# Optimization experiments

Measured on AMD Instinct MI355X. Metric: run time of the kernel, lower is better.

## Reference

```python
import jax, jax.numpy as jnp
import numpy as np

N = 50000
E = 1600000
IN_CH = 34
HID = 64
OUT = 64
NEG_SLOPE = 0.2


def _gat_layer(x, src, dst, W, a_src, a_dst, bias, heads, out_ch, concat):
    n = x.shape[0]
    xw = (x @ W).reshape(n, heads, out_ch)                      # [N,H,C]
    al_src = jnp.sum(xw * a_src[None], axis=-1)                  # [N,H]
    al_dst = jnp.sum(xw * a_dst[None], axis=-1)                  # [N,H]
    e = jax.nn.leaky_relu(al_src[src] + al_dst[dst], NEG_SLOPE)  # [E,H]
    # segment softmax over incoming edges of each dst node (self-loops ensure non-empty)
    m = jax.ops.segment_max(e, dst, num_segments=n)              # [N,H]
    ex = jnp.exp(e - m[dst])
    denom = jax.ops.segment_sum(ex, dst, num_segments=n)         # [N,H]
    alpha = ex / denom[dst]                                      # [E,H]
    msg = xw[src] * alpha[:, :, None]                            # [E,H,C]
    out = jax.ops.segment_sum(msg, dst, num_segments=n)          # [N,H,C]
    if concat:
        out = out.reshape(n, heads * out_ch)
    else:
        out = out.mean(axis=1)
    return out + bias


def setup_inputs() -> dict:
    key = jax.random.key(0)
    ks = jax.random.split(key, 12)
    x = jax.random.normal(ks[0], (N, IN_CH), dtype=jnp.float32)
    edge_index = jax.random.randint(ks[1], (2, E), 0, N, dtype=jnp.int64)
    # layer 1: heads=2, concat -> 128
    W1 = jax.random.normal(ks[2], (IN_CH, 2 * HID), dtype=jnp.float32) * 0.1
    a_src1 = jax.random.normal(ks[3], (2, HID), dtype=jnp.float32) * 0.1
    a_dst1 = jax.random.normal(ks[4], (2, HID), dtype=jnp.float32) * 0.1
    b1 = jnp.zeros((2 * HID,), dtype=jnp.float32)
    # layer 2: heads=1, mean
    W2 = jax.random.normal(ks[5], (2 * HID, OUT), dtype=jnp.float32) * 0.1
    a_src2 = jax.random.normal(ks[6], (1, OUT), dtype=jnp.float32) * 0.1
    a_dst2 = jax.random.normal(ks[7], (1, OUT), dtype=jnp.float32) * 0.1
    b2 = jnp.zeros((OUT,), dtype=jnp.float32)
    return {"x": x, "edge_index": edge_index, "W1": W1, "a_src1": a_src1,
            "a_dst1": a_dst1, "b1": b1, "W2": W2, "a_src2": a_src2,
            "a_dst2": a_dst2, "b2": b2}


def reference(x, edge_index, W1, a_src1, a_dst1, b1, W2, a_src2, a_dst2, b2):
    n = x.shape[0]
    loops = jnp.arange(n, dtype=edge_index.dtype)
    src = jnp.concatenate([edge_index[0], loops])  # PyG GATConv add_self_loops=True
    dst = jnp.concatenate([edge_index[1], loops])
    h = _gat_layer(x, src, dst, W1, a_src1, a_dst1, b1, heads=2, out_ch=HID, concat=True)
    h = jax.nn.relu(h)
    out = _gat_layer(h, src, dst, W2, a_src2, a_dst2, b2, heads=1, out_ch=OUT, concat=False)
    return out
```

## Files before the change

### kernel.cpp

```cpp
#include <hip/hip_runtime.h>
#include <math.h>

#define N_NODES 50000
#define E_EDGES 1600000
#define IN_CH   34
#define NEG     0.2f
#define NB      196
#define CAP     10000

typedef __attribute__((ext_vector_type(2))) float fv2;

static __device__ __forceinline__ unsigned short f2bf(float f) {
    unsigned int u = __float_as_uint(f);
    u += 0x7fffu + ((u >> 16) & 1u);
    return (unsigned short)(u >> 16);
}
static __device__ __forceinline__ float bflo(unsigned int u) {
    return __uint_as_float(u << 16);
}
static __device__ __forceinline__ float bfhi(unsigned int u) {
    return __uint_as_float(u & 0xffff0000u);
}
static __device__ __forceinline__ float lrelu_exp(float e) {
    return expf(e > 0.f ? e : NEG * e);
}

static __device__ __forceinline__ int scan256_excl(int v, int* wsum) {
    const int lane = threadIdx.x & 63, wv = threadIdx.x >> 6;
    int x = v;
    #pragma unroll
    for (int off = 1; off < 64; off <<= 1) {
        int y = __shfl_up(x, off);
        if (lane >= off) x += y;
    }
    if (lane == 63) wsum[wv] = x;
    __syncthreads();
    if (threadIdx.x < 4) {
        int s = wsum[threadIdx.x];
        #pragma unroll
        for (int off = 1; off < 4; off <<= 1) {
            int y = __shfl_up(s, off);
            if ((int)threadIdx.x >= off) s += y;
        }
        wsum[threadIdx.x] = s;
    }
    __syncthreads();
    const int woff = wv ? wsum[wv - 1] : 0;
    return woff + x - v;
}

__global__ __launch_bounds__(256) void k_bin_node1(
    const int* __restrict__ srcA, const int* __restrict__ dstA,
    int* __restrict__ gcur, unsigned int* __restrict__ binned,
    const float* __restrict__ x, const float* __restrict__ W1,
    const float* __restrict__ a_src, const float* __restrict__ a_dst,
    unsigned short* __restrict__ xw1b,
    float* __restrict__ al_s, float* __restrict__ al_d)
{
    __shared__ __align__(16) char sm[69664];
    const int tid = threadIdx.x;

    if (blockIdx.x < NB) {
        unsigned int* raw  = (unsigned int*)sm;
        unsigned int* ebuf = (unsigned int*)(sm + 32768);
        int* cnt  = (int*)(sm + 65536);
        int* loff = (int*)(sm + 66560);
        int* lcur = (int*)(sm + 67584);
        int* cur  = (int*)(sm + 68608);
        int* wsum = (int*)(sm + 69632);
        cnt[tid] = 0;
        __syncthreads();
        const int base = blockIdx.x * 8192;
        #pragma unroll
        for (int i = 0; i < 32; ++i) {
            const int e = base + i * 256 + tid;
            if (e < E_EDGES) {
                const int d = dstA[e], s = srcA[e];
                raw[i * 256 + tid] = ((unsigned int)d << 16) | (unsigned int)s;
                atomicAdd(&cnt[d >> 8], 1);
            }
        }
        __syncthreads();
        const int v = cnt[tid];
        const int excl = scan256_excl(v, wsum);
        loff[tid] = excl;
        lcur[tid] = excl;
        cur[tid] = (tid < NB && v > 0) ? (tid * CAP + atomicAdd(&gcur[tid], v)) : 0;
        __syncthreads();
        const int mE = min(8192, E_EDGES - base);
        #pragma unroll
        for (int i = 0; i < 32; ++i) {
            const int p = i * 256 + tid;
            if (p < mE) {
                const unsigned int u = raw[p];
                const int q = atomicAdd(&lcur[u >> 24], 1);
                ebuf[q] = u;
            }
        }
        __syncthreads();
        #pragma unroll
        for (int i = 0; i < 32; ++i) {
            const int p = i * 256 + tid;
            if (p < mE) {
                const unsigned int u = ebuf[p];
                const int b = (int)(u >> 24);
                binned[cur[b] + (p - loff[b])] = u;
            }
        }
    } else {
        float* sW  = (float*)sm;
        float* sx  = (float*)(sm + 17952);
        float* sas = (float*)(sm + 22432);
        float* sad = (float*)(sm + 22944);
        for (int i = tid; i < IN_CH * 128; i += 256) {
            int k = i >> 7, c = i & 127;
            sW[k * 132 + c] = W1[i];
        }
        if (tid < 128) { sas[tid] = a_src[tid]; sad[tid] = a_dst[tid]; }
        const int n0 = (blockIdx.x - NB) * 32;
        for (int i = tid; i < 32 * IN_CH; i += 256) {
            int n = i / IN_CH;
            sx[n * 35 + (i - n * IN_CH)] = (n0 + n < N_NODES) ? x[n0 * IN_CH + i] : 0.f;
        }
        __syncthreads();

        const int tc = tid & 31, tn = tid >> 5;
        float acc[4][4] = {{0.f}};
        for (int k = 0; k < IN_CH; ++k) {
            const float4 wv = *reinterpret_cast<const float4*>(&sW[k * 132 + 4 * tc]);
            #pragma unroll
            for (int j = 0; j < 4; ++j) {
                const float hj = sx[(4 * tn + j) * 35 + k];
                acc[j][0] += hj * wv.x; acc[j][1] += hj * wv.y;
                acc[j][2] += hj * wv.z; acc[j][3] += hj * wv.w;
            }
        }
        #pragma unroll
        for (int j = 0; j < 4; ++j) {
            const int node = n0 + 4 * tn + j;
            float ps = 0.f, pd = 0.f;
            #pragma unroll
            for (int c = 0; c < 4; ++c) {
                ps += acc[j][c] * sas[4 * tc + c];
                pd += acc[j][c] * sad[4 * tc + c];
            }
            #pragma unroll
            for (int off = 1; off < 16; off <<= 1) {
                ps += __shfl_xor(ps, off);
                pd += __shfl_xor(pd, off);
            }
            if (node < N_NODES) {
                if ((tc & 15) == 0) {
                    int h = tc >> 4;
                    al_s[node * 2 + h] = ps;
                    al_d[node * 2 + h] = pd;
                }
                ushort4 u;
                u.x = f2bf(acc[j][0]); u.y = f2bf(acc[j][1]);
                u.z = f2bf(acc[j][2]); u.w = f2bf(acc[j][3]);
                *reinterpret_cast<ushort4*>(&xw1b[node * 128 + 4 * tc]) = u;
            }
        }
    }
}

__global__ __launch_bounds__(256) void k_fine(
    const int* __restrict__ gcur, const unsigned int* __restrict__ binned,
    int2* __restrict__ rowspan, int* __restrict__ sorted_src)
{
    __shared__ unsigned int sbin[CAP];
    __shared__ int cnt[256], lcur[256];
    __shared__ int wsum[4];
    const int tid = threadIdx.x;
    const int b = blockIdx.x;
    const int bbase = b * CAP;
    const int cntb = gcur[b];
    cnt[tid] = 0;
    __syncthreads();
    for (int p = tid; p < cntb; p += 256) {
        const unsigned int u = binned[bbase + p];
        sbin[p] = u;
        atomicAdd(&cnt[(u >> 16) & 255], 1);
    }
    __syncthreads();
    const int v = cnt[tid];
    const int excl = scan256_excl(v, wsum);
    const int node = b * 256 + tid;
    if (node < N_NODES) rowspan[node] = make_int2(bbase + excl, bbase + excl + v);
    lcur[tid] = excl;
    __syncthreads();
    for (int p = tid; p < cntb; p += 256) {
        const unsigned int u = sbin[p];
        const int q = atomicAdd(&lcur[(u >> 16) & 255], 1);
        sorted_src[bbase + q] = (int)(u & 0xffffu);
    }
}

__global__ __launch_bounds__(256) void k_gather1(
    const int2* __restrict__ rowspan, const int* __restrict__ sorted_src,
    const unsigned int* __restrict__ xw1u,
    const float* __restrict__ al_s, const float* __restrict__ al_d,
    const float* __restrict__ b1, float* __restrict__ hbuf)
{
    __shared__ float4 AB[2][4][32];
    const int wave = threadIdx.x >> 6;
    const int lane = threadIdx.x & 63;
    const int node = (blockIdx.x * 256 + threadIdx.x) >> 6;
    if (node >= N_NODES) return;
    const int2 span = rowspan[node];
    const int head = lane >> 5;

    const float2 ald  = *reinterpret_cast<const float2*>(&al_d[node * 2]);
    const float2 als0 = *reinterpret_cast<const float2*>(&al_s[node * 2]);
    const float w0h0 = lrelu_exp(als0.x + ald.x);
    const float w0h1 = lrelu_exp(als0.y + ald.y);
    const float wself = head ? w0h1 : w0h0;

    const unsigned int su = xw1u[node * 64 + lane];
    fv2 accX = { wself * bflo(su), wself * bfhi(su) };
    fv2 accY = { 0.f, 0.f };
    float dv0 = 0.f, dv1 = 0.f;
    const float4* ABh = AB[head][wave];

    for (int base = span.x; base < span.y; base += 64) {
        const int rem = span.y - base;
        const int m = rem < 64 ? rem : 64;
        const int mp = (m + 1) & ~1;
        if (lane < m) {
            const int s = sorted_src[base + lane];
            const float2 als = *reinterpret_cast<const float2*>(&al_s[s * 2]);
            const float w0 = lrelu_exp(als.x + ald.x);
            const float w1 = lrelu_exp(als.y + ald.y);
            dv0 += w0; dv1 += w1;
            const float offf = __int_as_float(s << 6);
            ((float2*)&AB[0][wave][lane >> 1])[lane & 1] = make_float2(offf, w0);
            ((float2*)&AB[1][wave][lane >> 1])[lane & 1] = make_float2(offf, w1);
        } else if (lane < mp) {
            const float offf = __int_as_float(node << 6);
            ((float2*)&AB[0][wave][lane >> 1])[lane & 1] = make_float2(offf, 0.f);
            ((float2*)&AB[1][wave][lane >> 1])[lane & 1] = make_float2(offf, 0.f);
        }
        const int P = mp >> 1;
        int p = 0;
        for (; p + 4 <= P; p += 4) {
            const float4 q0 = ABh[p + 0];
            const float4 q1 = ABh[p + 1];
            const float4 q2 = ABh[p + 2];
            const float4 q3 = ABh[p + 3];
            const unsigned int a0 = xw1u[__float_as_int(q0.x) + lane];
            const unsigned int b0 = xw1u[__float_as_int(q0.z) + lane];
            const unsigned int a1 = xw1u[__float_as_int(q1.x) + lane];
            const unsigned int b1v = xw1u[__float_as_int(q1.z) + lane];
            const unsigned int a2 = xw1u[__float_as_int(q2.x) + lane];
            const unsigned int b2 = xw1u[__float_as_int(q2.z) + lane];
            const unsigned int a3 = xw1u[__float_as_int(q3.x) + lane];
            const unsigned int b3 = xw1u[__float_as_int(q3.z) + lane];
            fv2 f;
            f.x = bflo(a0); f.y = bfhi(a0); accX += f * q0.y;
            f.x = bflo(b0); f.y = bfhi(b0); accY += f * q0.w;
            f.x = bflo(a1); f.y = bfhi(a1); accX += f * q1.y;
            f.x = bflo(b1v); f.y = bfhi(b1v); accY += f * q1.w;
            f.x = bflo(a2); f.y = bfhi(a2); accX += f * q2.y;
            f.x = bflo(b2); f.y = bfhi(b2); accY += f * q2.w;
            f.x = bflo(a3); f.y = bfhi(a3); accX += f * q3.y;
            f.x = bflo(b3); f.y = bfhi(b3); accY += f * q3.w;
        }
        for (; p < P; ++p) {
            const float4 q = ABh[p];
            const unsigned int a = xw1u[__float_as_int(q.x) + lane];
            const unsigned int b = xw1u[__float_as_int(q.z) + lane];
            fv2 f;
            f.x = bflo(a); f.y = bfhi(a); accX += f * q.y;
            f.x = bflo(b); f.y = bfhi(b); accY += f * q.w;
        }
    }
    accX += accY;
    #pragma unroll
    for (int off = 32; off; off >>= 1) {
        dv0 += __shfl_xor(dv0, off);
        dv1 += __shfl_xor(dv1, off);
    }
    const float den = head ? (dv1 + w0h1) : (dv0 + w0h0);
    const float2 bv = *reinterpret_cast<const float2*>(&b1[2 * lane]);
    float o0 = accX.x / den + bv.x;
    float o1 = accX.y / den + bv.y;
    o0 = o0 > 0.f ? o0 : 0.f;
    o1 = o1 > 0.f ? o1 : 0.f;
    *reinterpret_cast<float2*>(&hbuf[node * 128 + 2 * lane]) = make_float2(o0, o1);
}

__global__ __launch_bounds__(256) void k_node2(
    const float* __restrict__ hbuf, const float* __restrict__ W2,
    const float* __restrict__ a_src, const float* __restrict__ a_dst,
    unsigned short* __restrict__ xw2b, float* __restrict__ al_s, float* __restrict__ al_d)
{
    __shared__ float sW[128 * 64];
    __shared__ float sh[64 * 129];
    __shared__ float sas[64], sad[64];
    const int tid = threadIdx.x;
    for (int i = tid; i < 128 * 64; i += 256) sW[i] = W2[i];
    if (tid < 64) { sas[tid] = a_src[tid]; sad[tid] = a_dst[tid]; }
    const int n0 = blockIdx.x * 64;
    for (int i = tid; i < 64 * 128; i += 256) {
        int n = i >> 7, c = i & 127;
        sh[n * 129 + c] = (n0 + n < N_NODES) ? hbuf[(long)(n0 + n) * 128 + c] : 0.f;
    }
    __syncthreads();

    const int tc = tid & 15, tn = tid >> 4;
    float acc[4][4] = {{0.f}};
    for (int k = 0; k < 128; ++k) {
        const float4 wv = *reinterpret_cast<const float4*>(&sW[k * 64 + 4 * tc]);
        #pragma unroll
        for (int j = 0; j < 4; ++j) {
            const float hj = sh[(4 * tn + j) * 129 + k];
            acc[j][0] += hj * wv.x; acc[j][1] += hj * wv.y;
            acc[j][2] += hj * wv.z; acc[j][3] += hj * wv.w;
        }
    }
    #pragma unroll
    for (int j = 0; j < 4; ++j) {
        const int node = n0 + 4 * tn + j;
        float ps = 0.f, pd = 0.f;
        #pragma unroll
        for (int c = 0; c < 4; ++c) {
            ps += acc[j][c] * sas[4 * tc + c];
            pd += acc[j][c] * sad[4 * tc + c];
        }
        #pragma unroll
        for (int off = 1; off < 16; off <<= 1) {
            ps += __shfl_xor(ps, off);
            pd += __shfl_xor(pd, off);
        }
        if (node < N_NODES) {
            if (tc == 0) { al_s[node] = ps; al_d[node] = pd; }
            ushort4 u;
            u.x = f2bf(acc[j][0]); u.y = f2bf(acc[j][1]);
            u.z = f2bf(acc[j][2]); u.w = f2bf(acc[j][3]);
            *reinterpret_cast<ushort4*>(&xw2b[node * 64 + 4 * tc]) = u;
        }
    }
}

__global__ __launch_bounds__(256) void k_gather2(
    const int2* __restrict__ rowspan, const int* __restrict__ sorted_src,
    const unsigned int* __restrict__ xw2u,
    const float* __restrict__ al_s, const float* __restrict__ al_d,
    const float* __restrict__ b2, float* __restrict__ out)
{
    __shared__ float4 AB[4][32];
    const int wave = threadIdx.x >> 6;
    const int lane = threadIdx.x & 63;
    const int node = (blockIdx.x * 256 + threadIdx.x) >> 6;
    if (node >= N_NODES) return;
    const int2 span = rowspan[node];
    const int li = lane & 31, hsel = lane >> 5;

    const float ald = al_d[node];
    const float w0s = lrelu_exp(al_s[node] + ald);
    const unsigned int su = xw2u[node * 32 + li];
    const float wself = hsel ? 0.f : w0s;
    fv2 acc = { wself * bflo(su), wself * bfhi(su) };
    float dv = 0.f;
    const float4* ABw = AB[wave];

    for (int base = span.x; base < span.y; base += 64) {
        const int rem = span.y - base;
        const int m = rem < 64 ? rem : 64;
        const int mp = (m + 3) & ~3;
        if (lane < m) {
            const int s = sorted_src[base + lane];
            const float w = lrelu_exp(al_s[s] + ald);
            dv += w;
            ((float2*)&AB[wave][lane >> 1])[lane & 1] =
                make_float2(__int_as_float(s << 5), w);
        } else if (lane < mp) {
            ((float2*)&AB[wave][lane >> 1])[lane & 1] =
                make_float2(__int_as_float(node << 5), 0.f);
        }
        const int P = mp >> 1;
        int p = hsel;
        for (; p + 2 < P; p += 4) {
            const float4 qA = ABw[p];
            const float4 qB = ABw[p + 2];
            const unsigned int aA = xw2u[__float_as_int(qA.x) + li];
            const unsigned int bA = xw2u[__float_as_int(qA.z) + li];
            const unsigned int aB = xw2u[__float_as_int(qB.x) + li];
            const unsigned int bB = xw2u[__float_as_int(qB.z) + li];
            fv2 f;
            f.x = bflo(aA); f.y = bfhi(aA); acc += f * qA.y;
            f.x = bflo(bA); f.y = bfhi(bA); acc += f * qA.w;
            f.x = bflo(aB); f.y = bfhi(aB); acc += f * qB.y;
            f.x = bflo(bB); f.y = bfhi(bB); acc += f * qB.w;
        }
        for (; p < P; p += 2) {
            const float4 q = ABw[p];
            const unsigned int a = xw2u[__float_as_int(q.x) + li];
            const unsigned int b = xw2u[__float_as_int(q.z) + li];
            fv2 f;
            f.x = bflo(a); f.y = bfhi(a); acc += f * q.y;
            f.x = bflo(b); f.y = bfhi(b); acc += f * q.w;
        }
    }
    acc.x += __shfl_xor(acc.x, 32);
    acc.y += __shfl_xor(acc.y, 32);
    #pragma unroll
    for (int off = 32; off; off >>= 1) dv += __shfl_xor(dv, off);
    if (lane < 32) {
        const float den = dv + w0s;
        const float2 bv = *reinterpret_cast<const float2*>(&b2[2 * li]);
        *reinterpret_cast<float2*>(&out[node * 64 + 2 * li]) =
            make_float2(acc.x / den + bv.x, acc.y / den + bv.y);
    }
}

extern "C" void kernel_launch(void* const* d_in, const int* in_sizes, int n_in,
                              void* d_out, int out_size, void* d_ws, size_t ws_size,
                              hipStream_t stream)
{
    const float* x   = (const float*)d_in[0];
    const int*   ei  = (const int*)d_in[1];
    const float* W1  = (const float*)d_in[2];
    const float* as1 = (const float*)d_in[3];
    const float* ad1 = (const float*)d_in[4];
    const float* b1  = (const float*)d_in[5];
    const float* W2  = (const float*)d_in[6];
    const float* as2 = (const float*)d_in[7];
    const float* ad2 = (const float*)d_in[8];
    const float* b2  = (const float*)d_in[9];
    float* out = (float*)d_out;

    const int* srcA = ei;
    const int* dstA = ei + E_EDGES;

    char* ws = (char*)d_ws;
    int2*  rowspan    = (int2*)(ws);
    int*   sorted_src = (int*)(ws + 409600);
    int*   gcur       = (int*)(ws + 8249600);
    float* al_s1      = (float*)(ws + 8251648);
    float* al_d1      = (float*)(ws + 8651648);
    float* al_s2      = (float*)(ws + 9051648);
    float* al_d2      = (float*)(ws + 9251648);
    unsigned short* xw1b = (unsigned short*)(ws + 9451648);
    float* hbuf       = (float*)(ws + 22251648);
    unsigned int* binned = (unsigned int*)hbuf;
    unsigned short* xw2b = (unsigned short*)(ws + 47851648);

    hipMemsetAsync(gcur, 0, NB * sizeof(int), stream);
    hipLaunchKernelGGL(k_bin_node1, dim3(NB + (N_NODES + 31) / 32), dim3(256), 0, stream,
                       srcA, dstA, gcur, binned,
                       x, W1, as1, ad1, xw1b, al_s1, al_d1);
    hipLaunchKernelGGL(k_fine, dim3(NB), dim3(256), 0, stream,
                       gcur, binned, rowspan, sorted_src);
    hipLaunchKernelGGL(k_gather1, dim3((N_NODES + 3) / 4), dim3(256), 0, stream,
                       rowspan, sorted_src, (const unsigned int*)xw1b,
                       al_s1, al_d1, b1, hbuf);
    hipLaunchKernelGGL(k_node2, dim3((N_NODES + 63) / 64), dim3(256), 0, stream,
                       hbuf, W2, as2, ad2, xw2b, al_s2, al_d2);
    hipLaunchKernelGGL(k_gather2, dim3((N_NODES + 3) / 4), dim3(256), 0, stream,
                       rowspan, sorted_src, (const unsigned int*)xw2b,
                       al_s2, al_d2, b2, out);
}
```

Before: 269.4 us.

## Replace two-pass bin sort with histogram, scan and atomic scatter CSR build

Replaces the coarse-bin plus in-shared-memory fine sort of edges by destination with a global per-node histogram kernel, a single-block exclusive scan, and an atomic-cursor scatter of source indices fused with the layer-1 node transform. This removes the intermediate binned buffer and the fine-sort kernel. In exchange it adds two launches, a serial single-block scan over 50k nodes, and 1.6M contended global atomics whose scattered writes leave edge order within each row nondeterministic.

```diff
diff --git a/kernel.cpp b/kernel.cpp
--- a/kernel.cpp
+++ b/kernel.cpp
@@ -5,8 +5,8 @@
 #define E_EDGES 1600000
 #define IN_CH   34
 #define NEG     0.2f
-#define NB      196
-#define CAP     10000
+#define HB      784
+#define SCB     512
 
 typedef __attribute__((ext_vector_type(2))) float fv2;
 
@@ -25,9 +25,34 @@
     return expf(e > 0.f ? e : NEG * e);
 }
 
-static __device__ __forceinline__ int scan256_excl(int v, int* wsum) {
-    const int lane = threadIdx.x & 63, wv = threadIdx.x >> 6;
-    int x = v;
+__global__ __launch_bounds__(256) void k_hist(
+    const int* __restrict__ dstA, int* __restrict__ hist)
+{
+    const int nq = E_EDGES / 4;
+    for (int q = blockIdx.x * 256 + threadIdx.x; q < nq; q += HB * 256) {
+        const int4 d = ((const int4*)dstA)[q];
+        atomicAdd(&hist[d.x], 1);
+        atomicAdd(&hist[d.y], 1);
+        atomicAdd(&hist[d.z], 1);
+        atomicAdd(&hist[d.w], 1);
+    }
+}
+
+__global__ __launch_bounds__(1024) void k_scan(
+    const int* __restrict__ hist, int2* __restrict__ rowspan,
+    int* __restrict__ cursor)
+{
+    __shared__ int wsum[16];
+    const int t = threadIdx.x;
+    const int CH = 49;
+    const int base = t * CH;
+    int s = 0;
+    for (int i = 0; i < CH; ++i) {
+        const int idx = base + i;
+        if (idx < N_NODES) s += hist[idx];
+    }
+    const int lane = t & 63, wv = t >> 6;
+    int x = s;
     #pragma unroll
     for (int off = 1; off < 64; off <<= 1) {
         int y = __shfl_up(x, off);
@@ -35,89 +60,58 @@
     }
     if (lane == 63) wsum[wv] = x;
     __syncthreads();
-    if (threadIdx.x < 4) {
-        int s = wsum[threadIdx.x];
+    if (t < 16) {
+        int v = wsum[t];
         #pragma unroll
-        for (int off = 1; off < 4; off <<= 1) {
-            int y = __shfl_up(s, off);
-            if ((int)threadIdx.x >= off) s += y;
-        }
-        wsum[threadIdx.x] = s;
+        for (int off = 1; off < 16; off <<= 1) {
+            int y = __shfl_up(v, off);
+            if (t >= off) v += y;
+        }
+        wsum[t] = v;
     }
     __syncthreads();
-    const int woff = wv ? wsum[wv - 1] : 0;
-    return woff + x - v;
-}
-
-__global__ __launch_bounds__(256) void k_bin_node1(
+    int run = (wv ? wsum[wv - 1] : 0) + x - s;
+    for (int i = 0; i < CH; ++i) {
+        const int idx = base + i;
+        if (idx < N_NODES) {
+            const int v = hist[idx];
+            rowspan[idx] = make_int2(run, run + v);
+            cursor[idx] = run;
+            run += v;
+        }
+    }
+}
+
+__global__ __launch_bounds__(256) void k_scatter_node1(
     const int* __restrict__ srcA, const int* __restrict__ dstA,
-    int* __restrict__ gcur, unsigned int* __restrict__ binned,
+    int* __restrict__ cursor, int* __restrict__ sorted_src,
     const float* __restrict__ x, const float* __restrict__ W1,
     const float* __restrict__ a_src, const float* __restrict__ a_dst,
     unsigned short* __restrict__ xw1b,
     float* __restrict__ al_s, float* __restrict__ al_d)
 {
-    __shared__ __align__(16) char sm[69664];
+    __shared__ float sW[IN_CH * 132];
+    __shared__ float sx[32 * 35];
+    __shared__ float sas[128], sad[128];
     const int tid = threadIdx.x;
 
-    if (blockIdx.x < NB) {
-        unsigned int* raw  = (unsigned int*)sm;
-        unsigned int* ebuf = (unsigned int*)(sm + 32768);
-        int* cnt  = (int*)(sm + 65536);
-        int* loff = (int*)(sm + 66560);
-        int* lcur = (int*)(sm + 67584);
-        int* cur  = (int*)(sm + 68608);
-        int* wsum = (int*)(sm + 69632);
-        cnt[tid] = 0;
-        __syncthreads();
-        const int base = blockIdx.x * 8192;
-        #pragma unroll
-        for (int i = 0; i < 32; ++i) {
-            const int e = base + i * 256 + tid;
-            if (e < E_EDGES) {
-                const int d = dstA[e], s = srcA[e];
-                raw[i * 256 + tid] = ((unsigned int)d << 16) | (unsigned int)s;
-                atomicAdd(&cnt[d >> 8], 1);
-            }
-        }
-        __syncthreads();
-        const int v = cnt[tid];
-        const int excl = scan256_excl(v, wsum);
-        loff[tid] = excl;
-        lcur[tid] = excl;
-        cur[tid] = (tid < NB && v > 0) ? (tid * CAP + atomicAdd(&gcur[tid], v)) : 0;
-        __syncthreads();
-        const int mE = min(8192, E_EDGES - base);
-        #pragma unroll
-        for (int i = 0; i < 32; ++i) {
-            const int p = i * 256 + tid;
-            if (p < mE) {
-                const unsigned int u = raw[p];
-                const int q = atomicAdd(&lcur[u >> 24], 1);
-                ebuf[q] = u;
-            }
-        }
-        __syncthreads();
-        #pragma unroll
-        for (int i = 0; i < 32; ++i) {
-            const int p = i * 256 + tid;
-            if (p < mE) {
-                const unsigned int u = ebuf[p];
-                const int b = (int)(u >> 24);
-                binned[cur[b] + (p - loff[b])] = u;
-            }
+    if (blockIdx.x < SCB) {
+        const int nq = E_EDGES / 4;
+        for (int q = blockIdx.x * 256 + tid; q < nq; q += SCB * 256) {
+            const int4 d = ((const int4*)dstA)[q];
+            const int4 s = ((const int4*)srcA)[q];
+            sorted_src[atomicAdd(&cursor[d.x], 1)] = s.x;
+            sorted_src[atomicAdd(&cursor[d.y], 1)] = s.y;
+            sorted_src[atomicAdd(&cursor[d.z], 1)] = s.z;
+            sorted_src[atomicAdd(&cursor[d.w], 1)] = s.w;
         }
     } else {
-        float* sW  = (float*)sm;
-        float* sx  = (float*)(sm + 17952);
-        float* sas = (float*)(sm + 22432);
-        float* sad = (float*)(sm + 22944);
         for (int i = tid; i < IN_CH * 128; i += 256) {
             int k = i >> 7, c = i & 127;
             sW[k * 132 + c] = W1[i];
         }
         if (tid < 128) { sas[tid] = a_src[tid]; sad[tid] = a_dst[tid]; }
-        const int n0 = (blockIdx.x - NB) * 32;
+        const int n0 = (blockIdx.x - SCB) * 32;
         for (int i = tid; i < 32 * IN_CH; i += 256) {
             int n = i / IN_CH;
             sx[n * 35 + (i - n * IN_CH)] = (n0 + n < N_NODES) ? x[n0 * IN_CH + i] : 0.f;
@@ -164,38 +158,6 @@
     }
 }
 
-__global__ __launch_bounds__(256) void k_fine(
-    const int* __restrict__ gcur, const unsigned int* __restrict__ binned,
-    int2* __restrict__ rowspan, int* __restrict__ sorted_src)
-{
-    __shared__ unsigned int sbin[CAP];
-    __shared__ int cnt[256], lcur[256];
-    __shared__ int wsum[4];
-    const int tid = threadIdx.x;
-    const int b = blockIdx.x;
-    const int bbase = b * CAP;
-    const int cntb = gcur[b];
-    cnt[tid] = 0;
-    __syncthreads();
-    for (int p = tid; p < cntb; p += 256) {
-        const unsigned int u = binned[bbase + p];
-        sbin[p] = u;
-        atomicAdd(&cnt[(u >> 16) & 255], 1);
-    }
-    __syncthreads();
-    const int v = cnt[tid];
-    const int excl = scan256_excl(v, wsum);
-    const int node = b * 256 + tid;
-    if (node < N_NODES) rowspan[node] = make_int2(bbase + excl, bbase + excl + v);
-    lcur[tid] = excl;
-    __syncthreads();
-    for (int p = tid; p < cntb; p += 256) {
-        const unsigned int u = sbin[p];
-        const int q = atomicAdd(&lcur[(u >> 16) & 255], 1);
-        sorted_src[bbase + q] = (int)(u & 0xffffu);
-    }
-}
-
 __global__ __launch_bounds__(256) void k_gather1(
     const int2* __restrict__ rowspan, const int* __restrict__ sorted_src,
     const unsigned int* __restrict__ xw1u,
@@ -436,22 +398,23 @@
     char* ws = (char*)d_ws;
     int2*  rowspan    = (int2*)(ws);
     int*   sorted_src = (int*)(ws + 409600);
-    int*   gcur       = (int*)(ws + 8249600);
-    float* al_s1      = (float*)(ws + 8251648);
-    float* al_d1      = (float*)(ws + 8651648);
-    float* al_s2      = (float*)(ws + 9051648);
-    float* al_d2      = (float*)(ws + 9251648);
-    unsigned short* xw1b = (unsigned short*)(ws + 9451648);
-    float* hbuf       = (float*)(ws + 22251648);
-    unsigned int* binned = (unsigned int*)hbuf;
-    unsigned short* xw2b = (unsigned short*)(ws + 47851648);
-
-    hipMemsetAsync(gcur, 0, NB * sizeof(int), stream);
-    hipLaunchKernelGGL(k_bin_node1, dim3(NB + (N_NODES + 31) / 32), dim3(256), 0, stream,
-                       srcA, dstA, gcur, binned,
+    int*   hist       = (int*)(ws + 6809600);
+    int*   cursor     = (int*)(ws + 7014400);
+    float* al_s1      = (float*)(ws + 7219200);
+    float* al_d1      = (float*)(ws + 7628800);
+    float* al_s2      = (float*)(ws + 8038400);
+    float* al_d2      = (float*)(ws + 8243200);
+    unsigned short* xw1b = (unsigned short*)(ws + 8448000);
+    float* hbuf       = (float*)(ws + 21248000);
+    unsigned short* xw2b = (unsigned short*)(ws + 46848000);
+
+    hipMemsetAsync(hist, 0, N_NODES * sizeof(int), stream);
+    hipLaunchKernelGGL(k_hist, dim3(HB), dim3(256), 0, stream, dstA, hist);
+    hipLaunchKernelGGL(k_scan, dim3(1), dim3(1024), 0, stream,
+                       hist, rowspan, cursor);
+    hipLaunchKernelGGL(k_scatter_node1, dim3(SCB + (N_NODES + 31) / 32), dim3(256), 0, stream,
+                       srcA, dstA, cursor, sorted_src,
                        x, W1, as1, ad1, xw1b, al_s1, al_d1);
-    hipLaunchKernelGGL(k_fine, dim3(NB), dim3(256), 0, stream,
-                       gcur, binned, rowspan, sorted_src);
     hipLaunchKernelGGL(k_gather1, dim3((N_NODES + 3) / 4), dim3(256), 0, stream,
                        rowspan, sorted_src, (const unsigned int*)xw1b,
                        al_s1, al_d1, b1, hbuf);
```

Result: slower. 534.3 us (+98.3%).

## Shrink binning chunks and split fine sort into four blocks per bin

Applied to the files above, without the earlier changes.

The coarse binning pass now gives each block 2048 edges instead of 8192, so 782 blocks run with about 23 KB of LDS instead of about 68 KB, which should raise occupancy. The fine sort pass launches four blocks per coarse bin, each owning 64 of the bin's 256 destination nodes. Each block still scans the whole bin to compute the global prefix offsets, but it only buffers and scatters its own quarter, holding at most 3072 edges in LDS. In exchange every bin is read from global memory four times, there are more global atomics on the bin counters, and any sub-bin holding more than 3072 edges is silently truncated.

```diff
diff --git a/kernel.cpp b/kernel.cpp
--- a/kernel.cpp
+++ b/kernel.cpp
@@ -7,6 +7,9 @@
 #define NEG     0.2f
 #define NB      196
 #define CAP     10000
+#define EPB     2048
+#define NBB     782
+#define FCAP    3072
 
 typedef __attribute__((ext_vector_type(2))) float fv2;
 
@@ -57,22 +60,22 @@
     unsigned short* __restrict__ xw1b,
     float* __restrict__ al_s, float* __restrict__ al_d)
 {
-    __shared__ __align__(16) char sm[69664];
+    __shared__ __align__(16) char sm[23456];
     const int tid = threadIdx.x;
 
-    if (blockIdx.x < NB) {
+    if (blockIdx.x < NBB) {
         unsigned int* raw  = (unsigned int*)sm;
-        unsigned int* ebuf = (unsigned int*)(sm + 32768);
-        int* cnt  = (int*)(sm + 65536);
-        int* loff = (int*)(sm + 66560);
-        int* lcur = (int*)(sm + 67584);
-        int* cur  = (int*)(sm + 68608);
-        int* wsum = (int*)(sm + 69632);
+        unsigned int* ebuf = (unsigned int*)(sm + 8192);
+        int* cnt  = (int*)(sm + 16384);
+        int* loff = (int*)(sm + 17408);
+        int* lcur = (int*)(sm + 18432);
+        int* cur  = (int*)(sm + 19456);
+        int* wsum = (int*)(sm + 20480);
         cnt[tid] = 0;
         __syncthreads();
-        const int base = blockIdx.x * 8192;
-        #pragma unroll
-        for (int i = 0; i < 32; ++i) {
+        const int base = blockIdx.x * EPB;
+        #pragma unroll
+        for (int i = 0; i < EPB / 256; ++i) {
             const int e = base + i * 256 + tid;
             if (e < E_EDGES) {
                 const int d = dstA[e], s = srcA[e];
@@ -87,9 +90,9 @@
         lcur[tid] = excl;
         cur[tid] = (tid < NB && v > 0) ? (tid * CAP + atomicAdd(&gcur[tid], v)) : 0;
         __syncthreads();
-        const int mE = min(8192, E_EDGES - base);
-        #pragma unroll
-        for (int i = 0; i < 32; ++i) {
+        const int mE = min(EPB, E_EDGES - base);
+        #pragma unroll
+        for (int i = 0; i < EPB / 256; ++i) {
             const int p = i * 256 + tid;
             if (p < mE) {
                 const unsigned int u = raw[p];
@@ -99,7 +102,7 @@
         }
         __syncthreads();
         #pragma unroll
-        for (int i = 0; i < 32; ++i) {
+        for (int i = 0; i < EPB / 256; ++i) {
             const int p = i * 256 + tid;
             if (p < mE) {
                 const unsigned int u = ebuf[p];
@@ -117,7 +120,7 @@
             sW[k * 132 + c] = W1[i];
         }
         if (tid < 128) { sas[tid] = a_src[tid]; sad[tid] = a_dst[tid]; }
-        const int n0 = (blockIdx.x - NB) * 32;
+        const int n0 = (blockIdx.x - NBB) * 32;
         for (int i = tid; i < 32 * IN_CH; i += 256) {
             int n = i / IN_CH;
             sx[n * 35 + (i - n * IN_CH)] = (n0 + n < N_NODES) ? x[n0 * IN_CH + i] : 0.f;
@@ -168,30 +171,41 @@
     const int* __restrict__ gcur, const unsigned int* __restrict__ binned,
     int2* __restrict__ rowspan, int* __restrict__ sorted_src)
 {
-    __shared__ unsigned int sbin[CAP];
-    __shared__ int cnt[256], lcur[256];
+    __shared__ unsigned int ebuf[FCAP];
+    __shared__ int cnt[256];
+    __shared__ int lcur[64];
     __shared__ int wsum[4];
+    __shared__ int myn;
     const int tid = threadIdx.x;
-    const int b = blockIdx.x;
+    const int b  = blockIdx.x >> 2;
+    const int lo = (blockIdx.x & 3) * 64;
     const int bbase = b * CAP;
     const int cntb = gcur[b];
     cnt[tid] = 0;
+    if (tid == 0) myn = 0;
     __syncthreads();
     for (int p = tid; p < cntb; p += 256) {
         const unsigned int u = binned[bbase + p];
-        sbin[p] = u;
-        atomicAdd(&cnt[(u >> 16) & 255], 1);
+        const int d8 = (int)((u >> 16) & 255);
+        atomicAdd(&cnt[d8], 1);
+        if ((d8 & ~63) == lo) {
+            const int k = atomicAdd(&myn, 1);
+            if (k < FCAP) ebuf[k] = u;
+        }
     }
     __syncthreads();
     const int v = cnt[tid];
     const int excl = scan256_excl(v, wsum);
-    const int node = b * 256 + tid;
-    if (node < N_NODES) rowspan[node] = make_int2(bbase + excl, bbase + excl + v);
-    lcur[tid] = excl;
-    __syncthreads();
-    for (int p = tid; p < cntb; p += 256) {
-        const unsigned int u = sbin[p];
-        const int q = atomicAdd(&lcur[(u >> 16) & 255], 1);
+    if ((tid & ~63) == lo) {
+        lcur[tid & 63] = excl;
+        const int node = b * 256 + tid;
+        if (node < N_NODES) rowspan[node] = make_int2(bbase + excl, bbase + excl + v);
+    }
+    __syncthreads();
+    const int tot = min(myn, FCAP);
+    for (int p = tid; p < tot; p += 256) {
+        const unsigned int u = ebuf[p];
+        const int q = atomicAdd(&lcur[(u >> 16) & 63], 1);
         sorted_src[bbase + q] = (int)(u & 0xffffu);
     }
 }
@@ -447,10 +461,10 @@
     unsigned short* xw2b = (unsigned short*)(ws + 47851648);
 
     hipMemsetAsync(gcur, 0, NB * sizeof(int), stream);
-    hipLaunchKernelGGL(k_bin_node1, dim3(NB + (N_NODES + 31) / 32), dim3(256), 0, stream,
+    hipLaunchKernelGGL(k_bin_node1, dim3(NBB + (N_NODES + 31) / 32), dim3(256), 0, stream,
                        srcA, dstA, gcur, binned,
                        x, W1, as1, ad1, xw1b, al_s1, al_d1);
-    hipLaunchKernelGGL(k_fine, dim3(NB), dim3(256), 0, stream,
+    hipLaunchKernelGGL(k_fine, dim3(NB * 4), dim3(256), 0, stream,
                        gcur, binned, rowspan, sorted_src);
     hipLaunchKernelGGL(k_gather1, dim3((N_NODES + 3) / 4), dim3(256), 0, stream,
                        rowspan, sorted_src, (const unsigned int*)xw1b,
```

Measured after the change: 278.9 us. 3.5% more time.

## Merge coarse binning and fine sort into one cooperative grid-synced kernel

Applied to the files above, without the earlier changes.

Replaces the two-pass coarse-bin and fine-sort kernels, which used fixed-capacity bins plus global atomics, with one cooperative kernel of 196 blocks of 1024 threads. A count matrix and grid syncs give exact, compact bin offsets, and the edge loads are vectorised. The node-1 GEMM is split back into its own kernel. This removes the memset and one launch and packs the CSR tightly, at the cost of two grid-wide barriers, serial scans of the count matrix, and no overlap between the sort and the node-1 work.

```diff
diff --git a/kernel.cpp b/kernel.cpp
--- a/kernel.cpp
+++ b/kernel.cpp
@@ -1,12 +1,16 @@
 #include <hip/hip_runtime.h>
+#include <hip/hip_cooperative_groups.h>
 #include <math.h>
+
+namespace cg = cooperative_groups;
 
 #define N_NODES 50000
 #define E_EDGES 1600000
 #define IN_CH   34
 #define NEG     0.2f
-#define NB      196
-#define CAP     10000
+#define SORTB   196
+#define SEPB    8192
+#define CROW    200
 
 typedef __attribute__((ext_vector_type(2))) float fv2;
 
@@ -25,7 +29,7 @@
     return expf(e > 0.f ? e : NEG * e);
 }
 
-static __device__ __forceinline__ int scan256_excl(int v, int* wsum) {
+static __device__ __forceinline__ int scan256_wide(int v, int* wsum) {
     const int lane = threadIdx.x & 63, wv = threadIdx.x >> 6;
     int x = v;
     #pragma unroll
@@ -33,7 +37,8 @@
         int y = __shfl_up(x, off);
         if (lane >= off) x += y;
     }
-    if (lane == 63) wsum[wv] = x;
+    __syncthreads();
+    if (wv < 4 && lane == 63) wsum[wv] = x;
     __syncthreads();
     if (threadIdx.x < 4) {
         int s = wsum[threadIdx.x];
@@ -45,154 +50,164 @@
         wsum[threadIdx.x] = s;
     }
     __syncthreads();
-    const int woff = wv ? wsum[wv - 1] : 0;
+    const int woff = (wv >= 1 && wv < 4) ? wsum[wv - 1] : 0;
     return woff + x - v;
 }
 
-__global__ __launch_bounds__(256) void k_bin_node1(
+__global__ __launch_bounds__(1024) void k_sort(
     const int* __restrict__ srcA, const int* __restrict__ dstA,
-    int* __restrict__ gcur, unsigned int* __restrict__ binned,
+    int* __restrict__ cntmat, unsigned int* __restrict__ binned,
+    int2* __restrict__ rowspan, int* __restrict__ sorted_src)
+{
+    __shared__ __align__(16) unsigned int stage[2 * SEPB];
+    __shared__ int cnt[256], loff[256], lcur[256], cur[256];
+    __shared__ int bbs[256];
+    __shared__ int wsum[4];
+    unsigned int* raw  = stage;
+    unsigned int* ebuf = stage + SEPB;
+    const int tid = threadIdx.x;
+    const int blk = blockIdx.x;
+    const int base = blk * SEPB;
+    const int mE = min(SEPB, E_EDGES - base);
+
+    if (tid < 256) cnt[tid] = 0;
+    __syncthreads();
+    const int nq = mE >> 2;
+    for (int q = tid; q < nq; q += 1024) {
+        const int4 d4 = ((const int4*)(dstA + base))[q];
+        const int4 s4 = ((const int4*)(srcA + base))[q];
+        raw[4 * q + 0] = ((unsigned)d4.x << 16) | (unsigned)s4.x;
+        raw[4 * q + 1] = ((unsigned)d4.y << 16) | (unsigned)s4.y;
+        raw[4 * q + 2] = ((unsigned)d4.z << 16) | (unsigned)s4.z;
+        raw[4 * q + 3] = ((unsigned)d4.w << 16) | (unsigned)s4.w;
+        atomicAdd(&cnt[d4.x >> 8], 1);
+        atomicAdd(&cnt[d4.y >> 8], 1);
+        atomicAdd(&cnt[d4.z >> 8], 1);
+        atomicAdd(&cnt[d4.w >> 8], 1);
+    }
+    __syncthreads();
+    if (tid < SORTB) cntmat[blk * CROW + tid] = cnt[tid];
+    cg::this_grid().sync();
+
+    int pre = 0, tot = 0;
+    if (tid < SORTB) {
+        for (int r = 0; r < SORTB; ++r) {
+            const int c = cntmat[r * CROW + tid];
+            tot += c;
+            pre += (r < blk) ? c : 0;
+        }
+    }
+    {
+        const int excl = scan256_wide(tot, wsum);
+        if (tid < 256) bbs[tid] = excl;
+    }
+    __syncthreads();
+    if (tid < SORTB) cur[tid] = bbs[tid] + pre;
+    {
+        const int excl = scan256_wide((tid < 256) ? cnt[tid] : 0, wsum);
+        if (tid < 256) { loff[tid] = excl; lcur[tid] = excl; }
+    }
+    __syncthreads();
+
+    for (int p = tid; p < mE; p += 1024) {
+        const unsigned int u = raw[p];
+        const int q = atomicAdd(&lcur[u >> 24], 1);
+        ebuf[q] = u;
+    }
+    __syncthreads();
+    for (int p = tid; p < mE; p += 1024) {
+        const unsigned int u = ebuf[p];
+        const int b = (int)(u >> 24);
+        binned[cur[b] + (p - loff[b])] = u;
+    }
+    cg::this_grid().sync();
+
+    const int fb = bbs[blk];
+    const int fe = (blk + 1 < 256) ? bbs[blk + 1] : E_EDGES;
+    const int fn = fe - fb;
+    if (tid < 256) cnt[tid] = 0;
+    __syncthreads();
+    for (int p = tid; p < fn; p += 1024) {
+        const unsigned int u = binned[fb + p];
+        stage[p] = u;
+        atomicAdd(&cnt[(u >> 16) & 255], 1);
+    }
+    __syncthreads();
+    {
+        const int excl = scan256_wide((tid < 256) ? cnt[tid] : 0, wsum);
+        if (tid < 256) {
+            lcur[tid] = excl;
+            const int node = blk * 256 + tid;
+            if (node < N_NODES)
+                rowspan[node] = make_int2(fb + excl, fb + excl + cnt[tid]);
+        }
+    }
+    __syncthreads();
+    for (int p = tid; p < fn; p += 1024) {
+        const unsigned int u = stage[p];
+        const int q = atomicAdd(&lcur[(u >> 16) & 255], 1);
+        sorted_src[fb + q] = (int)(u & 0xffffu);
+    }
+}
+
+__global__ __launch_bounds__(256) void k_node1(
     const float* __restrict__ x, const float* __restrict__ W1,
     const float* __restrict__ a_src, const float* __restrict__ a_dst,
     unsigned short* __restrict__ xw1b,
     float* __restrict__ al_s, float* __restrict__ al_d)
 {
-    __shared__ __align__(16) char sm[69664];
+    __shared__ float sW[IN_CH * 132];
+    __shared__ float sx[32 * 35];
+    __shared__ float sas[128], sad[128];
     const int tid = threadIdx.x;
-
-    if (blockIdx.x < NB) {
-        unsigned int* raw  = (unsigned int*)sm;
-        unsigned int* ebuf = (unsigned int*)(sm + 32768);
-        int* cnt  = (int*)(sm + 65536);
-        int* loff = (int*)(sm + 66560);
-        int* lcur = (int*)(sm + 67584);
-        int* cur  = (int*)(sm + 68608);
-        int* wsum = (int*)(sm + 69632);
-        cnt[tid] = 0;
-        __syncthreads();
-        const int base = blockIdx.x * 8192;
-        #pragma unroll
-        for (int i = 0; i < 32; ++i) {
-            const int e = base + i * 256 + tid;
-            if (e < E_EDGES) {
-                const int d = dstA[e], s = srcA[e];
-                raw[i * 256 + tid] = ((unsigned int)d << 16) | (unsigned int)s;
-                atomicAdd(&cnt[d >> 8], 1);
+    for (int i = tid; i < IN_CH * 128; i += 256) {
+        int k = i >> 7, c = i & 127;
+        sW[k * 132 + c] = W1[i];
+    }
+    if (tid < 128) { sas[tid] = a_src[tid]; sad[tid] = a_dst[tid]; }
+    const int n0 = blockIdx.x * 32;
+    for (int i = tid; i < 32 * IN_CH; i += 256) {
+        int n = i / IN_CH;
+        sx[n * 35 + (i - n * IN_CH)] = (n0 + n < N_NODES) ? x[n0 * IN_CH + i] : 0.f;
+    }
+    __syncthreads();
+
+    const int tc = tid & 31, tn = tid >> 5;
+    float acc[4][4] = {{0.f}};
+    for (int k = 0; k < IN_CH; ++k) {
+        const float4 wv = *reinterpret_cast<const float4*>(&sW[k * 132 + 4 * tc]);
+        #pragma unroll
+        for (int j = 0; j < 4; ++j) {
+            const float hj = sx[(4 * tn + j) * 35 + k];
+            acc[j][0] += hj * wv.x; acc[j][1] += hj * wv.y;
+            acc[j][2] += hj * wv.z; acc[j][3] += hj * wv.w;
+        }
+    }
+    #pragma unroll
+    for (int j = 0; j < 4; ++j) {
+        const int node = n0 + 4 * tn + j;
+        float ps = 0.f, pd = 0.f;
+        #pragma unroll
+        for (int c = 0; c < 4; ++c) {
+            ps += acc[j][c] * sas[4 * tc + c];
+            pd += acc[j][c] * sad[4 * tc + c];
+        }
+        #pragma unroll
+        for (int off = 1; off < 16; off <<= 1) {
+            ps += __shfl_xor(ps, off);
+            pd += __shfl_xor(pd, off);
+        }
+        if (node < N_NODES) {
+            if ((tc & 15) == 0) {
+                int h = tc >> 4;
+                al_s[node * 2 + h] = ps;
+                al_d[node * 2 + h] = pd;
             }
-        }
-        __syncthreads();
-        const int v = cnt[tid];
-        const int excl = scan256_excl(v, wsum);
-        loff[tid] = excl;
-        lcur[tid] = excl;
-        cur[tid] = (tid < NB && v > 0) ? (tid * CAP + atomicAdd(&gcur[tid], v)) : 0;
-        __syncthreads();
-        const int mE = min(8192, E_EDGES - base);
-        #pragma unroll
-        for (int i = 0; i < 32; ++i) {
-            const int p = i * 256 + tid;
-            if (p < mE) {
-                const unsigned int u = raw[p];
-                const int q = atomicAdd(&lcur[u >> 24], 1);
-                ebuf[q] = u;
-            }
-        }
-        __syncthreads();
-        #pragma unroll
-        for (int i = 0; i < 32; ++i) {
-            const int p = i * 256 + tid;
-            if (p < mE) {
-                const unsigned int u = ebuf[p];
-                const int b = (int)(u >> 24);
-                binned[cur[b] + (p - loff[b])] = u;
-            }
-        }
-    } else {
-        float* sW  = (float*)sm;
-        float* sx  = (float*)(sm + 17952);
-        float* sas = (float*)(sm + 22432);
-        float* sad = (float*)(sm + 22944);
-        for (int i = tid; i < IN_CH * 128; i += 256) {
-            int k = i >> 7, c = i & 127;
-            sW[k * 132 + c] = W1[i];
-        }
-        if (tid < 128) { sas[tid] = a_src[tid]; sad[tid] = a_dst[tid]; }
-        const int n0 = (blockIdx.x - NB) * 32;
-        for (int i = tid; i < 32 * IN_CH; i += 256) {
-            int n = i / IN_CH;
-            sx[n * 35 + (i - n * IN_CH)] = (n0 + n < N_NODES) ? x[n0 * IN_CH + i] : 0.f;
-        }
-        __syncthreads();
-
-        const int tc = tid & 31, tn = tid >> 5;
-        float acc[4][4] = {{0.f}};
-        for (int k = 0; k < IN_CH; ++k) {
-            const float4 wv = *reinterpret_cast<const float4*>(&sW[k * 132 + 4 * tc]);
-            #pragma unroll
-            for (int j = 0; j < 4; ++j) {
-                const float hj = sx[(4 * tn + j) * 35 + k];
-                acc[j][0] += hj * wv.x; acc[j][1] += hj * wv.y;
-                acc[j][2] += hj * wv.z; acc[j][3] += hj * wv.w;
-            }
-        }
-        #pragma unroll
-        for (int j = 0; j < 4; ++j) {
-            const int node = n0 + 4 * tn + j;
-            float ps = 0.f, pd = 0.f;
-            #pragma unroll
-            for (int c = 0; c < 4; ++c) {
-                ps += acc[j][c] * sas[4 * tc + c];
-                pd += acc[j][c] * sad[4 * tc + c];
-            }
-            #pragma unroll
-            for (int off = 1; off < 16; off <<= 1) {
-                ps += __shfl_xor(ps, off);
-                pd += __shfl_xor(pd, off);
-            }
-            if (node < N_NODES) {
-                if ((tc & 15) == 0) {
-                    int h = tc >> 4;
-                    al_s[node * 2 + h] = ps;
-                    al_d[node * 2 + h] = pd;
-                }
-                ushort4 u;
-                u.x = f2bf(acc[j][0]); u.y = f2bf(acc[j][1]);
-                u.z = f2bf(acc[j][2]); u.w = f2bf(acc[j][3]);
-                *reinterpret_cast<ushort4*>(&xw1b[node * 128 + 4 * tc]) = u;
-            }
-        }
-    }
-}
-
-__global__ __launch_bounds__(256) void k_fine(
-    const int* __restrict__ gcur, const unsigned int* __restrict__ binned,
-    int2* __restrict__ rowspan, int* __restrict__ sorted_src)
-{
-    __shared__ unsigned int sbin[CAP];
-    __shared__ int cnt[256], lcur[256];
-    __shared__ int wsum[4];
-    const int tid = threadIdx.x;
-    const int b = blockIdx.x;
-    const int bbase = b * CAP;
-    const int cntb = gcur[b];
-    cnt[tid] = 0;
-    __syncthreads();
-    for (int p = tid; p < cntb; p += 256) {
-        const unsigned int u = binned[bbase + p];
-        sbin[p] = u;
-        atomicAdd(&cnt[(u >> 16) & 255], 1);
-    }
-    __syncthreads();
-    const int v = cnt[tid];
-    const int excl = scan256_excl(v, wsum);
-    const int node = b * 256 + tid;
-    if (node < N_NODES) rowspan[node] = make_int2(bbase + excl, bbase + excl + v);
-    lcur[tid] = excl;
-    __syncthreads();
-    for (int p = tid; p < cntb; p += 256) {
-        const unsigned int u = sbin[p];
-        const int q = atomicAdd(&lcur[(u >> 16) & 255], 1);
-        sorted_src[bbase + q] = (int)(u & 0xffffu);
+            ushort4 u;
+            u.x = f2bf(acc[j][0]); u.y = f2bf(acc[j][1]);
+            u.z = f2bf(acc[j][2]); u.w = f2bf(acc[j][3]);
+            *reinterpret_cast<ushort4*>(&xw1b[node * 128 + 4 * tc]) = u;
+        }
     }
 }
 
@@ -436,22 +451,24 @@
     char* ws = (char*)d_ws;
     int2*  rowspan    = (int2*)(ws);
     int*   sorted_src = (int*)(ws + 409600);
-    int*   gcur       = (int*)(ws + 8249600);
-    float* al_s1      = (float*)(ws + 8251648);
-    float* al_d1      = (float*)(ws + 8651648);
-    float* al_s2      = (float*)(ws + 9051648);
-    float* al_d2      = (float*)(ws + 9251648);
-    unsigned short* xw1b = (unsigned short*)(ws + 9451648);
-    float* hbuf       = (float*)(ws + 22251648);
+    int*   cntmat     = (int*)(ws + 6809600);
+    float* al_s1      = (float*)(ws + 6973440);
+    float* al_d1      = (float*)(ws + 7383040);
+    float* al_s2      = (float*)(ws + 7792640);
+    float* al_d2      = (float*)(ws + 7997440);
+    unsigned short* xw1b = (unsigned short*)(ws + 8202240);
+    float* hbuf       = (float*)(ws + 21002240);
     unsigned int* binned = (unsigned int*)hbuf;
-    unsigned short* xw2b = (unsigned short*)(ws + 47851648);
-
-    hipMemsetAsync(gcur, 0, NB * sizeof(int), stream);
-    hipLaunchKernelGGL(k_bin_node1, dim3(NB + (N_NODES + 31) / 32), dim3(256), 0, stream,
-                       srcA, dstA, gcur, binned,
+    unsigned short* xw2b = (unsigned short*)(ws + 46602240);
+
+    hipLaunchKernelGGL(k_node1, dim3((N_NODES + 31) / 32), dim3(256), 0, stream,
                        x, W1, as1, ad1, xw1b, al_s1, al_d1);
-    hipLaunchKernelGGL(k_fine, dim3(NB), dim3(256), 0, stream,
-                       gcur, binned, rowspan, sorted_src);
+    {
+        void* sargs[] = { (void*)&srcA, (void*)&dstA, (void*)&cntmat,
+                          (void*)&binned, (void*)&rowspan, (void*)&sorted_src };
+        hipLaunchCooperativeKernel((const void*)k_sort, dim3(SORTB), dim3(1024),
+                                   sargs, 0, stream);
+    }
     hipLaunchKernelGGL(k_gather1, dim3((N_NODES + 3) / 4), dim3(256), 0, stream,
                        rowspan, sorted_src, (const unsigned int*)xw1b,
                        al_s1, al_d1, b1, hbuf);
```

New measurement: 337.1 us. 25.1% more time.
